# Optimization experiments

Measured on AMD Instinct MI355X. Metric: run time of the kernel, lower is better.

The kernel has to match this reference:

```python
import jax, jax.numpy as jnp
import numpy as np

B, T, C, H = 2, 2048, 1024, 16
D = C // H  # head dim = 64
EPS = 1e-5


def _layernorm(x, g, b):
    mu = jnp.mean(x, axis=-1, keepdims=True)
    var = jnp.mean((x - mu) ** 2, axis=-1, keepdims=True)
    return (x - mu) * jax.lax.rsqrt(var + EPS) * g + b


def setup_inputs() -> dict:
    key = jax.random.key(0)
    ks = jax.random.split(key, 16)
    s = 1.0 / np.sqrt(C)
    inp = {
        "x": jax.random.normal(ks[0], (B, T, C), dtype=jnp.float32),
        "Wq": jax.random.normal(ks[1], (C, C), dtype=jnp.float32) * s,
        "bq": jnp.zeros((C,), jnp.float32),
        "Wk": jax.random.normal(ks[2], (C, C), dtype=jnp.float32) * s,
        "bk": jnp.zeros((C,), jnp.float32),
        "Wv": jax.random.normal(ks[3], (C, C), dtype=jnp.float32) * s,
        "bv": jnp.zeros((C,), jnp.float32),
        "Wo": jax.random.normal(ks[4], (C, C), dtype=jnp.float32) * s,
        "bo": jnp.zeros((C,), jnp.float32),
        "ln1_g": jnp.ones((C,), jnp.float32),
        "ln1_b": jnp.zeros((C,), jnp.float32),
        "ln2_g": jnp.ones((C,), jnp.float32),
        "ln2_b": jnp.zeros((C,), jnp.float32),
        "W1": jax.random.normal(ks[5], (C, 4 * C), dtype=jnp.float32) * s,
        "b1": jnp.zeros((4 * C,), jnp.float32),
        "W2": jax.random.normal(ks[6], (4 * C, C), dtype=jnp.float32) * (1.0 / np.sqrt(4 * C)),
        "b2": jnp.zeros((C,), jnp.float32),
    }
    return inp


def _block(x, Wq, bq, Wk, bk, Wv, bv, Wo, bo, ln1_g, ln1_b, ln2_g, ln2_b, W1, b1, W2, b2):
    # --- attention sublayer (pre-LN, residual) ---
    h = _layernorm(x, ln1_g, ln1_b)
    q = (h @ Wq + bq).reshape(B, T, H, D)
    k = (h @ Wk + bk).reshape(B, T, H, D)
    v = (h @ Wv + bv).reshape(B, T, H, D)
    scores = jnp.einsum("bthd,bshd->bhts", q, k) * (1.0 / np.sqrt(D))
    attn = jax.nn.softmax(scores, axis=-1)  # dropout is identity at eval
    y = jnp.einsum("bhts,bshd->bthd", attn, v).reshape(B, T, C)
    x = x + (y @ Wo + bo)
    # --- MLP sublayer (pre-LN, residual) ---
    h2 = _layernorm(x, ln2_g, ln2_b)
    m = jax.nn.gelu(h2 @ W1 + b1, approximate=False)  # torch nn.GELU() is exact erf
    x = x + (m @ W2 + b2)
    return x


def reference(x, Wq, bq, Wk, bk, Wv, bv, Wo, bo, ln1_g, ln1_b, ln2_g, ln2_b, W1, b1, W2, b2):
    return _block(x, Wq, bq, Wk, bk, Wv, bv, Wo, bo, ln1_g, ln1_b, ln2_g, ln2_b, W1, b1, W2, b2)
```

## Files before the change

### kernel.cpp

```cpp
#include <hip/hip_runtime.h>
#include <math.h>

typedef unsigned short u16;
typedef unsigned int   u32;
using bf16x8 = __attribute__((ext_vector_type(8))) short;
using f32x4  = __attribute__((ext_vector_type(4))) float;
using f32x16 = __attribute__((ext_vector_type(16))) float;

static constexpr int Bb = 2, Tt = 2048, Cc = 1024, Hh = 16, Dd = 64;
static constexpr int QS = 3072;

__device__ __forceinline__ u16 f2bf(float f){
  u32 u = __builtin_bit_cast(u32, f);
  u += 0x7fffu + ((u >> 16) & 1u);
  return (u16)(u >> 16);
}

__device__ __forceinline__ void gl2lds16(const void* g, void* l){
  __builtin_amdgcn_global_load_lds((const __attribute__((address_space(1))) void*)g,
                                   (__attribute__((address_space(3))) void*)l, 16, 0, 0);
}

template<int N> __device__ __forceinline__ void waitvm(){
  if constexpr (N == 0) asm volatile("s_waitcnt vmcnt(0)" ::: "memory");
  else if constexpr (N == 4) asm volatile("s_waitcnt vmcnt(4)" ::: "memory");
  else if constexpr (N == 6) asm volatile("s_waitcnt vmcnt(6)" ::: "memory");
  else if constexpr (N == 8) asm volatile("s_waitcnt vmcnt(8)" ::: "memory");
}

__device__ __forceinline__ void barrier_pin(){
  __builtin_amdgcn_s_barrier();
  __builtin_amdgcn_sched_barrier(0);
}

__device__ __forceinline__ f32x4 mfma16(bf16x8 a, bf16x8 b, f32x4 c){
  return __builtin_amdgcn_mfma_f32_16x16x32_bf16(a, b, c, 0, 0, 0);
}
__device__ __forceinline__ f32x16 mfma32(bf16x8 a, bf16x8 b, f32x16 c){
  return __builtin_amdgcn_mfma_f32_32x32x16_bf16(a, b, c, 0, 0, 0);
}

__device__ __forceinline__ float exp2f_fast(float x){
#if __has_builtin(__builtin_amdgcn_exp2f)
  return __builtin_amdgcn_exp2f(x);
#else
  return __expf(x * 0.69314718056f);
#endif
}

__device__ __forceinline__ float gelu_f(float x){
  return 0.5f * x * (1.0f + erff(x * 0.70710678118654752f));
}

__device__ __forceinline__ void plane_swap(u32& a, u32& b){
  asm("v_permlane32_swap_b32 %0, %1" : "+v"(a), "+v"(b));
}
__device__ __forceinline__ u32 cvtpk_bf16(float lo, float hi){
  u32 r;
  asm("v_cvt_pk_bf16_f32 %0, %1, %2" : "=v"(r) : "v"(lo), "v"(hi));
  return r;
}

__global__ __launch_bounds__(256) void ln_kernel(const float* __restrict__ x,
    const float* __restrict__ g, const float* __restrict__ b, u16* __restrict__ out)
{
  int row = blockIdx.x;
  int tid = threadIdx.x;
  const float4* xr = (const float4*)(x + (size_t)row * Cc);
  float4 v = xr[tid];
  float s  = v.x + v.y + v.z + v.w;
  float s2 = v.x*v.x + v.y*v.y + v.z*v.z + v.w*v.w;
  #pragma unroll
  for (int off = 1; off < 64; off <<= 1){ s += __shfl_xor(s, off); s2 += __shfl_xor(s2, off); }
  __shared__ float red[8];
  int wid = tid >> 6;
  if ((tid & 63) == 0){ red[wid] = s; red[4 + wid] = s2; }
  __syncthreads();
  s  = red[0] + red[1] + red[2] + red[3];
  s2 = red[4] + red[5] + red[6] + red[7];
  float mu   = s * (1.0f / Cc);
  float var  = s2 * (1.0f / Cc) - mu * mu;
  float rstd = rsqrtf(var + 1e-5f);
  const float4 gg = ((const float4*)g)[tid];
  const float4 bb = ((const float4*)b)[tid];
  ushort4 o;
  o.x = f2bf((v.x - mu) * rstd * gg.x + bb.x);
  o.y = f2bf((v.y - mu) * rstd * gg.y + bb.y);
  o.z = f2bf((v.z - mu) * rstd * gg.z + bb.z);
  o.w = f2bf((v.w - mu) * rstd * gg.w + bb.w);
  *(ushort4*)(out + (size_t)row * Cc + tid * 4) = o;
}

__global__ __launch_bounds__(256) void transpose_cast_kernel(const float* __restrict__ in,
    u16* __restrict__ out, int R, int Ccols)
{
  __shared__ float tile[32][33];
  int tx = threadIdx.x, ty = threadIdx.y;
  int c0 = blockIdx.x * 32, r0 = blockIdx.y * 32;
  #pragma unroll
  for (int j = 0; j < 4; j++) tile[ty + j*8][tx] = in[(size_t)(r0 + ty + j*8) * Ccols + c0 + tx];
  __syncthreads();
  #pragma unroll
  for (int j = 0; j < 4; j++) out[(size_t)(c0 + ty + j*8) * R + r0 + tx] = f2bf(tile[tx][ty + j*8]);
}

__global__ __launch_bounds__(256) void transpose4_kernel(
    const float* __restrict__ s0, const float* __restrict__ s1,
    const float* __restrict__ s2, const float* __restrict__ s3,
    u16* __restrict__ d0, u16* __restrict__ d1, u16* __restrict__ d2, u16* __restrict__ d3)
{
  __shared__ float tile[32][33];
  int z = blockIdx.z;
  const float* in = (z == 0) ? s0 : (z == 1) ? s1 : (z == 2) ? s2 : s3;
  u16* out        = (z == 0) ? d0 : (z == 1) ? d1 : (z == 2) ? d2 : d3;
  int tx = threadIdx.x, ty = threadIdx.y;
  int c0 = blockIdx.x * 32, r0 = blockIdx.y * 32;
  #pragma unroll
  for (int j = 0; j < 4; j++) tile[ty + j*8][tx] = in[(size_t)(r0 + ty + j*8) * 1024 + c0 + tx];
  __syncthreads();
  #pragma unroll
  for (int j = 0; j < 4; j++) out[(size_t)(c0 + ty + j*8) * 1024 + r0 + tx] = f2bf(tile[tx][ty + j*8]);
}

__global__ __launch_bounds__(256) void pack3_kernel(const float* __restrict__ a,
    const float* __restrict__ b, const float* __restrict__ c, float* __restrict__ o)
{
  int i = blockIdx.x * 256 + threadIdx.x;
  float v = (i < 1024) ? a[i] : (i < 2048 ? b[i - 1024] : c[i - 2048]);
  o[i] = v;
}

__global__ __launch_bounds__(256) void transpose_v_kernel(const u16* __restrict__ v, u16* __restrict__ vt)
{
  __shared__ u16 tile[32][33];
  int tx = threadIdx.x, ty = threadIdx.y;
  int bh = blockIdx.z; int b = bh >> 4, h = bh & 15;
  int t0 = blockIdx.x * 32, d0 = blockIdx.y * 32;
  const u16* src = v + (size_t)b * Tt * QS + h * Dd;
  #pragma unroll
  for (int j = 0; j < 4; j++) tile[ty + j*8][tx] = src[(size_t)(t0 + ty + j*8) * QS + d0 + tx];
  __syncthreads();
  u16* dst = vt + (size_t)bh * Dd * Tt;
  #pragma unroll
  for (int j = 0; j < 4; j++) dst[(size_t)(d0 + ty + j*8) * Tt + t0 + tx] = tile[tx][ty + j*8];
}

template<int BM, int BN, int WM, int WN, int WPEU, int EPI>
__global__ __launch_bounds__(WM * WN * 64, WPEU) void gemmc_kernel(
    const u16* __restrict__ A, const u16* __restrict__ BT,
    const float* __restrict__ bias, const float* __restrict__ resid,
    void* __restrict__ out, int K, int ldA, int ldOut)
{
  constexpr int THREADS = WM * WN * 64;
  constexpr int MF = (BM / WM) / 16;
  constexpr int NF = (BN / WN) / 16;
  constexpr int AG = (BM * 8) / THREADS;
  constexpr int BG = (BN * 8) / THREADS;
  constexpr int NLOADS = AG + BG;

  __shared__ alignas(16) u16 As[2][BM * 64];
  __shared__ alignas(16) u16 Bs[2][BN * 64];

  const int tid  = threadIdx.x;
  const int lane = tid & 63, wid = tid >> 6;
  const int l15  = lane & 15, lg = lane >> 4;

  const int gx  = gridDim.x;
  const int lin = blockIdx.x + gx * blockIdx.y;
  const int nwg = gx * gridDim.y;
  const int wl  = (lin & 7) * (nwg >> 3) + (lin >> 3);
  const int rowBase = (wl % gx) * BM, colBase = (wl / gx) * BN;

  const int wr = wid / WN, wc = wid % WN;

  f32x4 acc[MF][NF] = {};

  auto stage = [&](int buf, int k0){
    #pragma unroll
    for (int j = 0; j < AG; j++){
      int g = tid + THREADS * j;
      int row = g >> 3, ch = (g & 7) ^ (row & 7);
      gl2lds16(A + (size_t)(rowBase + row) * ldA + k0 + ch * 8,
               (u16*)As[buf] + (wid * 64 + THREADS * j) * 8);
    }
    #pragma unroll
    for (int j = 0; j < BG; j++){
      int g = tid + THREADS * j;
      int row = g >> 3, ch = (g & 7) ^ (row & 7);
      gl2lds16(BT + (size_t)(colBase + row) * K + k0 + ch * 8,
               (u16*)Bs[buf] + (wid * 64 + THREADS * j) * 8);
    }
  };

  stage(0, 0);
  const int nt = K >> 6;
  int cur = 0;
  for (int t = 0; t < nt; ++t, cur ^= 1){
    if (t + 1 < nt){ stage(cur ^ 1, (t + 1) << 6); waitvm<NLOADS>(); }
    else           { waitvm<0>(); }
    __builtin_amdgcn_s_barrier();
    __builtin_amdgcn_sched_barrier(0);

    const u16* Asb = (const u16*)As[cur];
    const u16* Bsb = (const u16*)Bs[cur];

    bf16x8 bfr[NF][2];
    #pragma unroll
    for (int ni = 0; ni < NF; ni++){
      int r = wc * (BN / WN) + ni * 16 + l15;
      bfr[ni][0] = *(const bf16x8*)(Bsb + r * 64 + ((lg       ^ (r & 7)) << 3));
      bfr[ni][1] = *(const bf16x8*)(Bsb + r * 64 + (((4 + lg) ^ (r & 7)) << 3));
    }
    #pragma unroll
    for (int mi = 0; mi < MF; mi++){
      int r = wr * (BM / WM) + mi * 16 + l15;
      bf16x8 a0 = *(const bf16x8*)(Asb + r * 64 + ((lg       ^ (r & 7)) << 3));
      bf16x8 a1 = *(const bf16x8*)(Asb + r * 64 + (((4 + lg) ^ (r & 7)) << 3));
      __builtin_amdgcn_s_setprio(1);
      #pragma unroll
      for (int ni = 0; ni < NF; ni++){
        acc[mi][ni] = mfma16(a0, bfr[ni][0], acc[mi][ni]);
        acc[mi][ni] = mfma16(a1, bfr[ni][1], acc[mi][ni]);
      }
      __builtin_amdgcn_s_setprio(0);
    }

    __builtin_amdgcn_sched_barrier(0);
    __builtin_amdgcn_s_barrier();
  }

  #pragma unroll
  for (int mi = 0; mi < MF; mi++){
    #pragma unroll
    for (int ni = 0; ni < NF; ni++){
      int row = rowBase + wr * (BM / WM) + mi * 16 + lg * 4;
      int col = colBase + wc * (BN / WN) + ni * 16 + l15;
      float bc = bias[col];
      #pragma unroll
      for (int r = 0; r < 4; r++){
        float val = acc[mi][ni][r] + bc;
        size_t idx = (size_t)(row + r) * ldOut + col;
        if constexpr (EPI == 0)      ((u16*)out)[idx]   = f2bf(val);
        else if constexpr (EPI == 1) ((float*)out)[idx] = val + resid[idx];
        else                         ((u16*)out)[idx]   = f2bf(gelu_f(val));
      }
    }
  }
}

__global__ __launch_bounds__(256) void attn_kernel(const u16* __restrict__ q, const u16* __restrict__ k,
    const u16* __restrict__ vt, u16* __restrict__ y)
{
  __shared__ alignas(16) u16 Ks[2][64 * 64];
  __shared__ alignas(16) u16 Vs[2][64 * 64];
  int tid  = threadIdx.x;
  int lane = tid & 63, wid = tid >> 6;
  int l31  = lane & 31, hi = lane >> 5;

  int lin = blockIdx.x + 16 * blockIdx.y;
  int wl  = (lin & 7) * 64 + (lin >> 3);
  int qt  = wl & 15, bh = wl >> 4;
  int b = bh >> 4, h = bh & 15;

  int qglob = qt * 128 + wid * 32 + l31;

  const u16* qp = q + ((size_t)b * Tt + qglob) * QS + h * Dd + hi * 8;
  bf16x8 qf[4];
  #pragma unroll
  for (int s = 0; s < 4; s++) qf[s] = *(const bf16x8*)(qp + s * 16);

  const u16* kbase = k  + (size_t)b * Tt * QS + h * Dd;
  const u16* vbase = vt + (size_t)bh * Dd * Tt;

  f32x16 yacc[2] = {};
  float m2 = -1e30f, lsum = 0.f;
  const float CL = 0.125f * 1.44269504089f;

  int g0 = tid, g1 = tid + 256;
  int r0 = g0 >> 3, cb0 = (g0 & 7) ^ (r0 & 7);
  int r1 = g1 >> 3, cb1 = (g1 & 7) ^ (r1 & 7);

  auto stageKV = [&](int buf, int kt){
    gl2lds16(kbase + (size_t)(kt + r0) * QS + cb0 * 8, (u16*)Ks[buf] + wid * 512);
    gl2lds16(kbase + (size_t)(kt + r1) * QS + cb1 * 8, (u16*)Ks[buf] + 2048 + wid * 512);
    gl2lds16(vbase + (size_t)r0 * Tt + kt + cb0 * 8,   (u16*)Vs[buf] + wid * 512);
    gl2lds16(vbase + (size_t)r1 * Tt + kt + cb1 * 8,   (u16*)Vs[buf] + 2048 + wid * 512);
  };

  stageKV(0, 0);
  int cur = 0;
  for (int kt = 0; kt < Tt; kt += 64) {
    if (kt + 64 < Tt) { stageKV(cur ^ 1, kt + 64); waitvm<4>(); }
    else              { waitvm<0>(); }
    barrier_pin();

    const u16* Ksb = (const u16*)Ks[cur];
    const u16* Vsb = (const u16*)Vs[cur];
    int rx = l31 & 7;

    f32x16 st[2] = {};
    __builtin_amdgcn_s_setprio(1);
    #pragma unroll
    for (int nb = 0; nb < 2; nb++){
      const u16* krow = Ksb + (nb * 32 + l31) * 64;
      #pragma unroll
      for (int s = 0; s < 4; s++){
        bf16x8 kf = *(const bf16x8*)(krow + (((s * 2 + hi) ^ rx) << 3));
        st[nb] = mfma32(kf, qf[s], st[nb]);
      }
    }
    __builtin_amdgcn_s_setprio(0);

    float tm[16];
    #pragma unroll
    for (int i = 0; i < 16; i++) tm[i] = fmaxf(st[0][i], st[1][i]);
    #pragma unroll
    for (int w = 8; w; w >>= 1)
      #pragma unroll
      for (int i = 0; i < w; i++) tm[i] = fmaxf(tm[i], tm[i + w]);
    u32 ma = __builtin_bit_cast(u32, tm[0]), mb = ma;
    plane_swap(ma, mb);
    float mx = fmaxf(__builtin_bit_cast(float, ma), __builtin_bit_cast(float, mb));
    float mnew = fmaxf(m2, mx * CL);
    float alpha = exp2f_fast(m2 - mnew);
    m2 = mnew;

    #pragma unroll
    for (int nb = 0; nb < 2; nb++)
      #pragma unroll
      for (int i = 0; i < 16; i++)
        st[nb][i] = exp2f_fast(st[nb][i] * CL - mnew);

    float ts[16];
    #pragma unroll
    for (int i = 0; i < 16; i++) ts[i] = st[0][i] + st[1][i];
    #pragma unroll
    for (int w = 8; w; w >>= 1)
      #pragma unroll
      for (int i = 0; i < w; i++) ts[i] += ts[i + w];
    u32 sa = __builtin_bit_cast(u32, ts[0]), sb = sa;
    plane_swap(sa, sb);
    float rs = __builtin_bit_cast(float, sa) + __builtin_bit_cast(float, sb);
    lsum = lsum * alpha + rs;

    #pragma unroll
    for (int nd = 0; nd < 2; nd++)
      #pragma unroll
      for (int i = 0; i < 16; i++) yacc[nd][i] *= alpha;

    bf16x8 pb[4];
    #pragma unroll
    for (int nb = 0; nb < 2; nb++){
      u32 c[8];
      #pragma unroll
      for (int i = 0; i < 8; i++) c[i] = cvtpk_bf16(st[nb][2 * i], st[nb][2 * i + 1]);
      plane_swap(c[0], c[2]); plane_swap(c[1], c[3]);
      plane_swap(c[4], c[6]); plane_swap(c[5], c[7]);
      u32 f0[4] = {c[0], c[1], c[2], c[3]};
      u32 f1[4] = {c[4], c[5], c[6], c[7]};
      pb[nb * 2 + 0] = *(bf16x8*)f0;
      pb[nb * 2 + 1] = *(bf16x8*)f1;
    }

    __builtin_amdgcn_s_setprio(1);
    #pragma unroll
    for (int nd = 0; nd < 2; nd++){
      const u16* vrow = Vsb + (nd * 32 + l31) * 64;
      #pragma unroll
      for (int ks = 0; ks < 4; ks++){
        bf16x8 vf = *(const bf16x8*)(vrow + (((ks * 2 + hi) ^ rx) << 3));
        yacc[nd] = mfma32(vf, pb[ks], yacc[nd]);
      }
    }
    __builtin_amdgcn_s_setprio(0);

    __builtin_amdgcn_sched_barrier(0);
    barrier_pin();
    cur ^= 1;
  }

  float inv = 1.0f / lsum;
  u16* yp = y + ((size_t)b * Tt + qt * 128 + wid * 32 + l31) * Cc + h * Dd;
  #pragma unroll
  for (int nd = 0; nd < 2; nd++){
    #pragma unroll
    for (int g = 0; g < 4; g++){
      ushort4 o;
      o.x = f2bf(yacc[nd][g * 4 + 0] * inv);
      o.y = f2bf(yacc[nd][g * 4 + 1] * inv);
      o.z = f2bf(yacc[nd][g * 4 + 2] * inv);
      o.w = f2bf(yacc[nd][g * 4 + 3] * inv);
      *(ushort4*)(yp + nd * 32 + g * 8 + hi * 4) = o;
    }
  }
}

extern "C" void kernel_launch(void* const* d_in, const int* in_sizes, int n_in,
                              void* d_out, int out_size, void* d_ws, size_t ws_size,
                              hipStream_t stream)
{
  (void)in_sizes; (void)n_in; (void)out_size; (void)ws_size;
  const float* x    = (const float*)d_in[0];
  const float* Wq   = (const float*)d_in[1];
  const float* bq   = (const float*)d_in[2];
  const float* Wk   = (const float*)d_in[3];
  const float* bk   = (const float*)d_in[4];
  const float* Wv   = (const float*)d_in[5];
  const float* bv   = (const float*)d_in[6];
  const float* Wo   = (const float*)d_in[7];
  const float* bo   = (const float*)d_in[8];
  const float* ln1g = (const float*)d_in[9];
  const float* ln1b = (const float*)d_in[10];
  const float* ln2g = (const float*)d_in[11];
  const float* ln2b = (const float*)d_in[12];
  const float* W1   = (const float*)d_in[13];
  const float* b1   = (const float*)d_in[14];
  const float* W2   = (const float*)d_in[15];
  const float* b2   = (const float*)d_in[16];

  char* ws = (char*)d_ws;
  const size_t MB = 1024 * 1024;
  u16*   wqkvt = (u16*)(ws + 0 * MB);
  u16*   wot   = (u16*)(ws + 6 * MB);
  u16*   w1t   = (u16*)(ws + 8 * MB);
  u16*   w2t   = (u16*)(ws + 16 * MB);
  float* bqkv  = (float*)(ws + 24 * MB);
  u16*   hbuf  = (u16*)(ws + 25 * MB);
  u16*   qkv   = (u16*)(ws + 33 * MB);
  u16*   vtb   = (u16*)(ws + 57 * MB);
  u16*   yb    = (u16*)(ws + 65 * MB);
  float* x2    = (float*)(ws + 73 * MB);
  u16*   h2    = hbuf;
  u16*   mb    = qkv;

  dim3 tb(32, 8);
  transpose4_kernel<<<dim3(32, 32, 4), tb, 0, stream>>>(Wq, Wk, Wv, Wo,
      wqkvt, wqkvt + 1024 * 1024, wqkvt + 2048 * 1024, wot);
  transpose_cast_kernel<<<dim3(128, 32), tb, 0, stream>>>(W1, w1t, 1024, 4096);
  transpose_cast_kernel<<<dim3(32, 128), tb, 0, stream>>>(W2, w2t, 4096, 1024);
  pack3_kernel<<<12, 256, 0, stream>>>(bq, bk, bv, bqkv);

  ln_kernel<<<4096, 256, 0, stream>>>(x, ln1g, ln1b, hbuf);

  gemmc_kernel<128, 128, 2, 2, 2, 0><<<dim3(32, 24), 256, 0, stream>>>(hbuf, wqkvt, bqkv, nullptr, qkv, 1024, 1024, 3072);

  transpose_v_kernel<<<dim3(64, 2, 32), tb, 0, stream>>>(qkv + 2048, vtb);

  attn_kernel<<<dim3(16, 32), 256, 0, stream>>>(qkv, qkv + 1024, vtb, yb);

  gemmc_kernel<64, 128, 2, 2, 3, 1><<<dim3(64, 8), 256, 0, stream>>>(yb, wot, bo, x, x2, 1024, 1024, 1024);

  ln_kernel<<<4096, 256, 0, stream>>>(x2, ln2g, ln2b, h2);

  gemmc_kernel<128, 128, 2, 2, 2, 2><<<dim3(32, 32), 256, 0, stream>>>(h2, w1t, b1, nullptr, mb, 1024, 1024, 4096);

  gemmc_kernel<64, 128, 2, 2, 3, 1><<<dim3(64, 8), 256, 0, stream>>>(mb, w2t, b2, x2, (float*)d_out, 4096, 4096, 1024);
}
```

Measured before the change: 275.4 us.

## Split attention over key halves with combine kernel; fold softmax scale into Q

The attention grid gains a second dimension that splits the key sequence into two halves. Each half writes partial bf16 outputs plus per-row max and sum, and a new combine kernel merges them into y. This doubles the number of attention blocks (512 to 1024) so more of the GPU's compute units are busy. The softmax scale and log2e factor move into the QKV GEMM epilogue for the Q columns, which removes a multiply per score. The cost is an extra kernel launch, partial-output traffic, and an extra bf16 rounding of the partial results.

```diff
diff --git a/kernel.cpp b/kernel.cpp
--- a/kernel.cpp
+++ b/kernel.cpp
@@ -9,11 +9,16 @@
 
 static constexpr int Bb = 2, Tt = 2048, Cc = 1024, Hh = 16, Dd = 64;
 static constexpr int QS = 3072;
+static constexpr float QSCALE = 0.125f * 1.44269504089f;
 
 __device__ __forceinline__ u16 f2bf(float f){
   u32 u = __builtin_bit_cast(u32, f);
   u += 0x7fffu + ((u >> 16) & 1u);
   return (u16)(u >> 16);
+}
+__device__ __forceinline__ float bf2f(u16 v){
+  u32 u = (u32)v << 16;
+  return __builtin_bit_cast(float, u);
 }
 
 __device__ __forceinline__ void gl2lds16(const void* g, void* l){
@@ -242,14 +247,15 @@
         size_t idx = (size_t)(row + r) * ldOut + col;
         if constexpr (EPI == 0)      ((u16*)out)[idx]   = f2bf(val);
         else if constexpr (EPI == 1) ((float*)out)[idx] = val + resid[idx];
-        else                         ((u16*)out)[idx]   = f2bf(gelu_f(val));
+        else if constexpr (EPI == 2) ((u16*)out)[idx]   = f2bf(gelu_f(val));
+        else                         ((u16*)out)[idx]   = f2bf(col < 1024 ? val * QSCALE : val);
       }
     }
   }
 }
 
-__global__ __launch_bounds__(256) void attn_kernel(const u16* __restrict__ q, const u16* __restrict__ k,
-    const u16* __restrict__ vt, u16* __restrict__ y)
+__global__ __launch_bounds__(256, 4) void attn_kernel(const u16* __restrict__ q, const u16* __restrict__ k,
+    const u16* __restrict__ vt, u16* __restrict__ opart, float* __restrict__ ml)
 {
   __shared__ alignas(16) u16 Ks[2][64 * 64];
   __shared__ alignas(16) u16 Vs[2][64 * 64];
@@ -261,6 +267,8 @@
   int wl  = (lin & 7) * 64 + (lin >> 3);
   int qt  = wl & 15, bh = wl >> 4;
   int b = bh >> 4, h = bh & 15;
+  int split = blockIdx.z;
+  int kt0 = split * (Tt / 2);
 
   int qglob = qt * 128 + wid * 32 + l31;
 
@@ -274,7 +282,6 @@
 
   f32x16 yacc[2] = {};
   float m2 = -1e30f, lsum = 0.f;
-  const float CL = 0.125f * 1.44269504089f;
 
   int g0 = tid, g1 = tid + 256;
   int r0 = g0 >> 3, cb0 = (g0 & 7) ^ (r0 & 7);
@@ -287,11 +294,11 @@
     gl2lds16(vbase + (size_t)r1 * Tt + kt + cb1 * 8,   (u16*)Vs[buf] + 2048 + wid * 512);
   };
 
-  stageKV(0, 0);
+  stageKV(0, kt0);
   int cur = 0;
-  for (int kt = 0; kt < Tt; kt += 64) {
-    if (kt + 64 < Tt) { stageKV(cur ^ 1, kt + 64); waitvm<4>(); }
-    else              { waitvm<0>(); }
+  for (int kt = kt0; kt < kt0 + Tt / 2; kt += 64) {
+    if (kt + 64 < kt0 + Tt / 2) { stageKV(cur ^ 1, kt + 64); waitvm<4>(); }
+    else                        { waitvm<0>(); }
     barrier_pin();
 
     const u16* Ksb = (const u16*)Ks[cur];
@@ -321,7 +328,8 @@
     u32 ma = __builtin_bit_cast(u32, tm[0]), mb = ma;
     plane_swap(ma, mb);
     float mx = fmaxf(__builtin_bit_cast(float, ma), __builtin_bit_cast(float, mb));
-    float mnew = fmaxf(m2, mx * CL);
+
+    float mnew = fmaxf(m2, mx);
     float alpha = exp2f_fast(m2 - mnew);
     m2 = mnew;
 
@@ -329,7 +337,7 @@
     for (int nb = 0; nb < 2; nb++)
       #pragma unroll
       for (int i = 0; i < 16; i++)
-        st[nb][i] = exp2f_fast(st[nb][i] * CL - mnew);
+        st[nb][i] = exp2f_fast(st[nb][i] - m2);
 
     float ts[16];
     #pragma unroll
@@ -340,8 +348,7 @@
       for (int i = 0; i < w; i++) ts[i] += ts[i + w];
     u32 sa = __builtin_bit_cast(u32, ts[0]), sb = sa;
     plane_swap(sa, sb);
-    float rs = __builtin_bit_cast(float, sa) + __builtin_bit_cast(float, sb);
-    lsum = lsum * alpha + rs;
+    lsum = lsum * alpha + __builtin_bit_cast(float, sa) + __builtin_bit_cast(float, sb);
 
     #pragma unroll
     for (int nd = 0; nd < 2; nd++)
@@ -380,7 +387,7 @@
   }
 
   float inv = 1.0f / lsum;
-  u16* yp = y + ((size_t)b * Tt + qt * 128 + wid * 32 + l31) * Cc + h * Dd;
+  u16* op = opart + ((size_t)split * (Bb * Tt) + (size_t)b * Tt + qglob) * Cc + h * Dd;
   #pragma unroll
   for (int nd = 0; nd < 2; nd++){
     #pragma unroll
@@ -390,9 +397,36 @@
       o.y = f2bf(yacc[nd][g * 4 + 1] * inv);
       o.z = f2bf(yacc[nd][g * 4 + 2] * inv);
       o.w = f2bf(yacc[nd][g * 4 + 3] * inv);
-      *(ushort4*)(yp + nd * 32 + g * 8 + hi * 4) = o;
+      *(ushort4*)(op + nd * 32 + g * 8 + hi * 4) = o;
     }
   }
+  if (hi == 0){
+    float* mlp = ml + (((size_t)split * (Bb * Tt) + (size_t)b * Tt + qglob) * Hh + h) * 2;
+    mlp[0] = m2; mlp[1] = lsum;
+  }
+}
+
+__global__ __launch_bounds__(256) void combine_kernel(const u16* __restrict__ opart,
+    const float* __restrict__ ml, u16* __restrict__ y)
+{
+  int row = blockIdx.x;
+  int d0  = threadIdx.x * 4;
+  int h   = d0 >> 6;
+  const float* p0 = ml + ((size_t)row * Hh + h) * 2;
+  const float* p1 = ml + (((size_t)(Bb * Tt) + row) * Hh + h) * 2;
+  float m0 = p0[0], l0 = p0[1], m1 = p1[0], l1 = p1[1];
+  float M  = fmaxf(m0, m1);
+  float u0 = l0 * exp2f_fast(m0 - M), u1 = l1 * exp2f_fast(m1 - M);
+  float inv = 1.0f / (u0 + u1);
+  float w0 = u0 * inv, w1 = u1 * inv;
+  ushort4 a = *(const ushort4*)(opart + (size_t)row * Cc + d0);
+  ushort4 c = *(const ushort4*)(opart + ((size_t)(Bb * Tt) + row) * Cc + d0);
+  ushort4 o;
+  o.x = f2bf(bf2f(a.x) * w0 + bf2f(c.x) * w1);
+  o.y = f2bf(bf2f(a.y) * w0 + bf2f(c.y) * w1);
+  o.z = f2bf(bf2f(a.z) * w0 + bf2f(c.z) * w1);
+  o.w = f2bf(bf2f(a.w) * w0 + bf2f(c.w) * w1);
+  *(ushort4*)(y + (size_t)row * Cc + d0) = o;
 }
 
 extern "C" void kernel_launch(void* const* d_in, const int* in_sizes, int n_in,
@@ -429,7 +463,9 @@
   u16*   qkv   = (u16*)(ws + 33 * MB);
   u16*   vtb   = (u16*)(ws + 57 * MB);
   u16*   yb    = (u16*)(ws + 65 * MB);
+  u16*   opart = (u16*)(ws + 73 * MB);
   float* x2    = (float*)(ws + 73 * MB);
+  float* mlb   = (float*)(ws + 89 * MB);
   u16*   h2    = hbuf;
   u16*   mb    = qkv;
 
@@ -442,11 +478,12 @@
 
   ln_kernel<<<4096, 256, 0, stream>>>(x, ln1g, ln1b, hbuf);
 
-  gemmc_kernel<128, 128, 2, 2, 2, 0><<<dim3(32, 24), 256, 0, stream>>>(hbuf, wqkvt, bqkv, nullptr, qkv, 1024, 1024, 3072);
+  gemmc_kernel<128, 128, 2, 2, 2, 3><<<dim3(32, 24), 256, 0, stream>>>(hbuf, wqkvt, bqkv, nullptr, qkv, 1024, 1024, 3072);
 
   transpose_v_kernel<<<dim3(64, 2, 32), tb, 0, stream>>>(qkv + 2048, vtb);
 
-  attn_kernel<<<dim3(16, 32), 256, 0, stream>>>(qkv, qkv + 1024, vtb, yb);
+  attn_kernel<<<dim3(16, 32, 2), 256, 0, stream>>>(qkv, qkv + 1024, vtb, opart, mlb);
+  combine_kernel<<<4096, 256, 0, stream>>>(opart, mlb, yb);
 
   gemmc_kernel<64, 128, 2, 2, 3, 1><<<dim3(64, 8), 256, 0, stream>>>(yb, wot, bo, x, x2, 1024, 1024, 1024);
 
```

Result: no change. 274.3 us (-0.4%).
